# Optimization experiments

Measured on AMD Instinct MI355X. Metric: run time of the kernel, lower is better.

The kernel has to match this reference:

```python
import jax, jax.numpy as jnp
import numpy as np

DROP_P = 0.5

def setup_inputs() -> dict:
    key = jax.random.key(0)
    k_x, k_q, k_k, k_v = jax.random.split(key, 4)
    T, d_in, d_out = 4096, 1024, 1024
    x = jax.random.normal(k_x, (T, d_in), dtype=jnp.float32)
    # torch nn.Linear weights are [d_out, d_in]; init scale ~ 1/sqrt(d_in)
    s = 1.0 / np.sqrt(d_in)
    W_query = jax.random.uniform(k_q, (d_out, d_in), jnp.float32, -s, s)
    W_key = jax.random.uniform(k_k, (d_out, d_in), jnp.float32, -s, s)
    W_value = jax.random.uniform(k_v, (d_out, d_in), jnp.float32, -s, s)
    return {"x": x, "W_query": W_query, "W_key": W_key, "W_value": W_value}


def reference(x, W_query, W_key, W_value):
    # QKV projections (y = x @ W.T, matching torch Linear)
    queries = x @ W_query.T          # [T, d]
    keys = x @ W_key.T               # [T, d]
    # values = x @ W_value.T  -> feeds only the unused context_vec; dead code omitted
    d = keys.shape[-1]
    T = x.shape[0]
    attn_scores = queries @ keys.T   # [T, T]
    attn_weights = jax.nn.softmax(attn_scores / jnp.sqrt(jnp.float32(d)), axis=-1)
    # post-softmax causal masking + row renormalization (as in source)
    row = jnp.arange(T)
    causal = (row[:, None] >= row[None, :]).astype(attn_weights.dtype)  # tril of ones
    masked = attn_weights * causal
    masked_norm = masked / jnp.sum(masked, axis=-1, keepdims=True)
    # dropout(p=0.5), train mode, fixed seed
    keep = jax.random.bernoulli(jax.random.key(123), 1.0 - DROP_P, masked_norm.shape)
    return jnp.where(keep, masked_norm / (1.0 - DROP_P), 0.0)
```

## Files before the change

kernel.cpp:

```cpp
#include <hip/hip_runtime.h>
#include <hip/hip_bf16.h>


using bf16   = __bf16;
using bf16x8 = __attribute__((ext_vector_type(8))) __bf16;
using bf16x4 = __attribute__((ext_vector_type(4))) __bf16;
using f32x4  = __attribute__((ext_vector_type(4))) float;

constexpr int Tdim = 4096;
constexpr int Ddim = 1024;

__global__ __launch_bounds__(256) void k_cast_bf16(const float* __restrict__ in,
                                                   bf16* __restrict__ out, int n4) {
  int i = blockIdx.x * 256 + threadIdx.x;
  if (i >= n4) return;
  f32x4 v = reinterpret_cast<const f32x4*>(in)[i];
  bf16x4 o;
  o[0] = (bf16)v[0]; o[1] = (bf16)v[1]; o[2] = (bf16)v[2]; o[3] = (bf16)v[3];
  reinterpret_cast<bf16x4*>(out)[i] = o;
}

template<int OUTF32>
__global__ __launch_bounds__(256)
void k_gemm_bt(const bf16* __restrict__ A, const bf16* __restrict__ B,
               void* __restrict__ Cv, int M, int N, int K, int causal) {
  const int nbn = N >> 7;
  const int bm = blockIdx.x / nbn;
  const int bn = blockIdx.x - bm * nbn;
  if (causal && bn > bm) return;

  __shared__ __align__(16) bf16 As[128 * 32];
  __shared__ __align__(16) bf16 Bs[128 * 32];

  const int tid  = threadIdx.x;
  const int lane = tid & 63;
  const int wid  = tid >> 6;
  const int wr   = (wid >> 1) * 64;
  const int wc   = (wid & 1) * 64;
  const int fr   = lane & 15;
  const int ko   = (lane >> 4) * 8;

  f32x4 acc[4][4];
#pragma unroll
  for (int i = 0; i < 4; ++i)
#pragma unroll
    for (int j = 0; j < 4; ++j) acc[i][j] = (f32x4){0.f, 0.f, 0.f, 0.f};

  const bf16* Ag = A + (long)bm * 128 * K;
  const bf16* Bg = B + (long)bn * 128 * K;

  const int srow0 = tid >> 2;
  const int scol  = (tid & 3) * 8;

  for (int kt = 0; kt < K; kt += 32) {
#pragma unroll
    for (int i = 0; i < 2; ++i) {
      const int row = i * 64 + srow0;
      const int ldsbase = (i * 256 + wid * 64) * 8;
      __builtin_amdgcn_global_load_lds(
          (const __attribute__((address_space(1))) void*)(Ag + (long)row * K + kt + scol),
          (__attribute__((address_space(3))) void*)(As + ldsbase), 16, 0, 0);
      __builtin_amdgcn_global_load_lds(
          (const __attribute__((address_space(1))) void*)(Bg + (long)row * K + kt + scol),
          (__attribute__((address_space(3))) void*)(Bs + ldsbase), 16, 0, 0);
    }
    __syncthreads();

    bf16x8 av[4], bv[4];
#pragma unroll
    for (int f = 0; f < 4; ++f) {
      av[f] = *reinterpret_cast<const bf16x8*>(&As[(wr + f * 16 + fr) * 32 + ko]);
      bv[f] = *reinterpret_cast<const bf16x8*>(&Bs[(wc + f * 16 + fr) * 32 + ko]);
    }
#pragma unroll
    for (int fm = 0; fm < 4; ++fm)
#pragma unroll
      for (int fn = 0; fn < 4; ++fn)
        acc[fm][fn] = __builtin_amdgcn_mfma_f32_16x16x32_bf16(av[fm], bv[fn], acc[fm][fn], 0, 0, 0);
    __syncthreads();
  }

  const int crow0 = (lane >> 4) * 4;
  const int ccol  = lane & 15;
#pragma unroll
  for (int fm = 0; fm < 4; ++fm)
#pragma unroll
    for (int fn = 0; fn < 4; ++fn)
#pragma unroll
      for (int j = 0; j < 4; ++j) {
        const long row = (long)bm * 128 + wr + fm * 16 + crow0 + j;
        const long col = (long)bn * 128 + wc + fn * 16 + ccol;
        const float v = acc[fm][fn][j];
        if (OUTF32) ((float*)Cv)[row * N + col] = v;
        else        ((bf16*)Cv)[row * N + col] = (bf16)v;
      }
}

__device__ __forceinline__ unsigned rotl32(unsigned v, int d) {
  return (v << d) | (v >> (32 - d));
}
__device__ __forceinline__ void threefry_123(unsigned x0, unsigned x1,
                                             unsigned& o0, unsigned& o1) {
  const unsigned ks0 = 0u, ks1 = 123u;
  const unsigned ks2 = 0x1BD11BDAu ^ ks0 ^ ks1;
  x0 += ks0; x1 += ks1;
#define TF_R4(a, b, c, d)                                   \
  x0 += x1; x1 = rotl32(x1, a); x1 ^= x0;                   \
  x0 += x1; x1 = rotl32(x1, b); x1 ^= x0;                   \
  x0 += x1; x1 = rotl32(x1, c); x1 ^= x0;                   \
  x0 += x1; x1 = rotl32(x1, d); x1 ^= x0;
  TF_R4(13, 15, 26, 6);  x0 += ks1; x1 += ks2 + 1u;
  TF_R4(17, 29, 16, 24); x0 += ks2; x1 += ks0 + 2u;
  TF_R4(13, 15, 26, 6);  x0 += ks0; x1 += ks1 + 3u;
  TF_R4(17, 29, 16, 24); x0 += ks1; x1 += ks2 + 4u;
  TF_R4(13, 15, 26, 6);  x0 += ks2; x1 += ks0 + 5u;
#undef TF_R4
  o0 = x0; o1 = x1;
}

__device__ __forceinline__ bool keep_bit(unsigned i) {
  unsigned o0, o1;
  threefry_123(0u, i, o0, o1);
  return ((o0 ^ o1) & 0x80000000u) == 0u;
}

__global__ __launch_bounds__(256) void k_softmax_drop(float* __restrict__ S) {
  const int b  = blockIdx.x;
  const int r0 = b, r1 = b + (Tdim / 2);
  const int tid = threadIdx.x;
  __shared__ float redA[4], redB[4];

  float v0[8], v1[16];
  float lm0 = -3.0e38f, lm1 = -3.0e38f;
#pragma unroll
  for (int i = 0; i < 8; ++i) {
    const int c = tid + i * 256;
    v0[i] = (c <= r0) ? S[(long)r0 * Tdim + c] : -3.0e38f;
    lm0 = fmaxf(lm0, v0[i]);
  }
#pragma unroll
  for (int i = 0; i < 16; ++i) {
    const int c = tid + i * 256;
    v1[i] = (c <= r1) ? S[(long)r1 * Tdim + c] : -3.0e38f;
    lm1 = fmaxf(lm1, v1[i]);
  }
#pragma unroll
  for (int o = 32; o; o >>= 1) {
    lm0 = fmaxf(lm0, __shfl_xor(lm0, o));
    lm1 = fmaxf(lm1, __shfl_xor(lm1, o));
  }
  if ((tid & 63) == 0) { redA[tid >> 6] = lm0; redB[tid >> 6] = lm1; }
  __syncthreads();
  const float m0 = fmaxf(fmaxf(redA[0], redA[1]), fmaxf(redA[2], redA[3]));
  const float m1 = fmaxf(fmaxf(redB[0], redB[1]), fmaxf(redB[2], redB[3]));
  __syncthreads();

  constexpr float SC = 1.0f / 32.0f;
  float ls0 = 0.f, ls1 = 0.f;
#pragma unroll
  for (int i = 0; i < 8; ++i) {
    const int c = tid + i * 256;
    const float e = (c <= r0) ? __expf((v0[i] - m0) * SC) : 0.f;
    v0[i] = e; ls0 += e;
  }
#pragma unroll
  for (int i = 0; i < 16; ++i) {
    const int c = tid + i * 256;
    const float e = (c <= r1) ? __expf((v1[i] - m1) * SC) : 0.f;
    v1[i] = e; ls1 += e;
  }
#pragma unroll
  for (int o = 32; o; o >>= 1) { ls0 += __shfl_xor(ls0, o); ls1 += __shfl_xor(ls1, o); }
  if ((tid & 63) == 0) { redA[tid >> 6] = ls0; redB[tid >> 6] = ls1; }
  __syncthreads();
  const float inv0 = 2.0f / (redA[0] + redA[1] + redA[2] + redA[3]);
  const float inv1 = 2.0f / (redB[0] + redB[1] + redB[2] + redB[3]);

#pragma unroll
  for (int i = 0; i < 16; ++i) {
    const int c = tid + i * 256;
    const unsigned j = (unsigned)(r0 * Tdim + c);
    float o1v = 0.f;
    if (c <= r1 && keep_bit(j + 8388608u)) o1v = v1[i] * inv1;
    S[(long)r1 * Tdim + c] = o1v;
    float o0v = 0.f;
    if (i < 8 && c <= r0 && keep_bit(j)) o0v = v0[i & 7] * inv0;
    S[(long)r0 * Tdim + c] = o0v;
  }
}

extern "C" void kernel_launch(void* const* d_in, const int* in_sizes, int n_in,
                              void* d_out, int out_size, void* d_ws, size_t ws_size,
                              hipStream_t stream) {
  const float* x  = (const float*)d_in[0];
  const float* Wq = (const float*)d_in[1];
  const float* Wk = (const float*)d_in[2];
  float* S  = (float*)d_out;
  char* ws  = (char*)d_ws;
  bf16* xb  = (bf16*)(ws);
  bf16* wqb = (bf16*)(ws + (8l  << 20));
  bf16* wkb = (bf16*)(ws + (10l << 20));
  bf16* Qb  = (bf16*)(ws + (12l << 20));
  bf16* Kb  = (bf16*)(ws + (20l << 20));

  k_cast_bf16<<<(Tdim * Ddim / 4) / 256, 256, 0, stream>>>(x,  xb,  Tdim * Ddim / 4);
  k_cast_bf16<<<(Ddim * Ddim / 4) / 256, 256, 0, stream>>>(Wq, wqb, Ddim * Ddim / 4);
  k_cast_bf16<<<(Ddim * Ddim / 4) / 256, 256, 0, stream>>>(Wk, wkb, Ddim * Ddim / 4);

  k_gemm_bt<0><<<(Tdim / 128) * (Ddim / 128), 256, 0, stream>>>(xb, wqb, Qb, Tdim, Ddim, Ddim, 0);
  k_gemm_bt<0><<<(Tdim / 128) * (Ddim / 128), 256, 0, stream>>>(xb, wkb, Kb, Tdim, Ddim, Ddim, 0);
  k_gemm_bt<1><<<(Tdim / 128) * (Tdim / 128), 256, 0, stream>>>(Qb, Kb, (void*)S, Tdim, Tdim, Ddim, 1);

  k_softmax_drop<<<Tdim / 2, 256, 0, stream>>>(S);
}
```

Measured before the change: 215.4 us.

## Reassociate QK^T via fused weight product Wq^T Wk and double-buffer GEMM LDS

Instead of projecting both Q and K from x, the launcher forms G = Wk^T Wq (a 1024x1024 product computed with split-K and a reduce-cast), then P = x G^T, and finally S = P x^T. This drops one T x D x D projection GEMM, replacing it with a cheaper D^3 product plus a transpose-cast and a reduction kernel. The GEMM kernel also gains double-buffered LDS staging so the next tile's global-to-LDS loads overlap the current tile's MFMAs. It costs extra launches and rounds the product to bf16 at one more point, which changes the rounding of the scores.

```diff
diff --git a/kernel.cpp b/kernel.cpp
--- a/kernel.cpp
+++ b/kernel.cpp
@@ -20,17 +20,57 @@
   reinterpret_cast<bf16x4*>(out)[i] = o;
 }
 
+__global__ __launch_bounds__(256) void k_tcast(const float* __restrict__ q,
+                                               const float* __restrict__ k,
+                                               bf16* __restrict__ qt,
+                                               bf16* __restrict__ kt) {
+  const float* in = blockIdx.z ? k : q;
+  bf16* out = blockIdx.z ? kt : qt;
+  __shared__ float t[32][33];
+  const int tx = threadIdx.x & 31;
+  const int ty = threadIdx.x >> 5;
+  const int r0 = blockIdx.y * 32;
+  const int c0 = blockIdx.x * 32;
+#pragma unroll
+  for (int r = 0; r < 4; ++r)
+    t[ty * 4 + r][tx] = in[(r0 + ty * 4 + r) * Ddim + c0 + tx];
+  __syncthreads();
+#pragma unroll
+  for (int r = 0; r < 4; ++r)
+    out[(c0 + ty * 4 + r) * Ddim + r0 + tx] = (bf16)t[tx][ty * 4 + r];
+}
+
+__global__ __launch_bounds__(256) void k_redcast(const float* __restrict__ p,
+                                                 bf16* __restrict__ g) {
+  const int i = blockIdx.x * 256 + threadIdx.x;
+  f32x4 a = reinterpret_cast<const f32x4*>(p)[i];
+  f32x4 b = reinterpret_cast<const f32x4*>(p + (1 << 20))[i];
+  f32x4 c = reinterpret_cast<const f32x4*>(p + (2 << 20))[i];
+  f32x4 d = reinterpret_cast<const f32x4*>(p + (3 << 20))[i];
+  f32x4 s = a + b + c + d;
+  bf16x4 o;
+  o[0] = (bf16)s[0]; o[1] = (bf16)s[1]; o[2] = (bf16)s[2]; o[3] = (bf16)s[3];
+  reinterpret_cast<bf16x4*>(g)[i] = o;
+}
+
+__device__ __forceinline__ void gll16(const bf16* g, bf16* l) {
+  __builtin_amdgcn_global_load_lds(
+      (const __attribute__((address_space(1))) void*)g,
+      (__attribute__((address_space(3))) void*)l, 16, 0, 0);
+}
+
 template<int OUTF32>
 __global__ __launch_bounds__(256)
 void k_gemm_bt(const bf16* __restrict__ A, const bf16* __restrict__ B,
-               void* __restrict__ Cv, int M, int N, int K, int causal) {
+               void* __restrict__ Cv, int N, int lda, int ldb, int kLen,
+               long cZs, int causal) {
   const int nbn = N >> 7;
   const int bm = blockIdx.x / nbn;
   const int bn = blockIdx.x - bm * nbn;
   if (causal && bn > bm) return;
 
-  __shared__ __align__(16) bf16 As[128 * 32];
-  __shared__ __align__(16) bf16 Bs[128 * 32];
+  __shared__ __align__(16) bf16 As[2][128 * 32];
+  __shared__ __align__(16) bf16 Bs[2][128 * 32];
 
   const int tid  = threadIdx.x;
   const int lane = tid & 63;
@@ -46,39 +86,45 @@
 #pragma unroll
     for (int j = 0; j < 4; ++j) acc[i][j] = (f32x4){0.f, 0.f, 0.f, 0.f};
 
-  const bf16* Ag = A + (long)bm * 128 * K;
-  const bf16* Bg = B + (long)bn * 128 * K;
-
+  const bf16* Ag = A + (long)bm * 128 * lda;
+  const bf16* Bg = B + (long)bn * 128 * ldb;
   const int srow0 = tid >> 2;
   const int scol  = (tid & 3) * 8;
-
-  for (int kt = 0; kt < K; kt += 32) {
+  const int k0 = blockIdx.y * kLen;
+
+  auto stage = [&](int buf, int kt) {
 #pragma unroll
     for (int i = 0; i < 2; ++i) {
       const int row = i * 64 + srow0;
-      const int ldsbase = (i * 256 + wid * 64) * 8;
-      __builtin_amdgcn_global_load_lds(
-          (const __attribute__((address_space(1))) void*)(Ag + (long)row * K + kt + scol),
-          (__attribute__((address_space(3))) void*)(As + ldsbase), 16, 0, 0);
-      __builtin_amdgcn_global_load_lds(
-          (const __attribute__((address_space(1))) void*)(Bg + (long)row * K + kt + scol),
-          (__attribute__((address_space(3))) void*)(Bs + ldsbase), 16, 0, 0);
+      const int lb  = (i * 256 + wid * 64) * 8;
+      gll16(Ag + (long)row * lda + kt + scol, &As[buf][lb]);
+      gll16(Bg + (long)row * ldb + kt + scol, &Bs[buf][lb]);
     }
-    __syncthreads();
-
+  };
+  auto compute = [&](int buf) {
     bf16x8 av[4], bv[4];
 #pragma unroll
     for (int f = 0; f < 4; ++f) {
-      av[f] = *reinterpret_cast<const bf16x8*>(&As[(wr + f * 16 + fr) * 32 + ko]);
-      bv[f] = *reinterpret_cast<const bf16x8*>(&Bs[(wc + f * 16 + fr) * 32 + ko]);
+      av[f] = *reinterpret_cast<const bf16x8*>(&As[buf][(wr + f * 16 + fr) * 32 + ko]);
+      bv[f] = *reinterpret_cast<const bf16x8*>(&Bs[buf][(wc + f * 16 + fr) * 32 + ko]);
     }
 #pragma unroll
     for (int fm = 0; fm < 4; ++fm)
 #pragma unroll
       for (int fn = 0; fn < 4; ++fn)
         acc[fm][fn] = __builtin_amdgcn_mfma_f32_16x16x32_bf16(av[fm], bv[fn], acc[fm][fn], 0, 0, 0);
+  };
+
+  stage(0, k0);
+  __syncthreads();
+  int cur = 0;
+  for (int kt = 32; kt < kLen; kt += 32) {
+    stage(cur ^ 1, k0 + kt);
+    compute(cur);
     __syncthreads();
-  }
+    cur ^= 1;
+  }
+  compute(cur);
 
   const int crow0 = (lane >> 4) * 4;
   const int ccol  = lane & 15;
@@ -91,7 +137,7 @@
         const long row = (long)bm * 128 + wr + fm * 16 + crow0 + j;
         const long col = (long)bn * 128 + wc + fn * 16 + ccol;
         const float v = acc[fm][fn][j];
-        if (OUTF32) ((float*)Cv)[row * N + col] = v;
+        if (OUTF32) ((float*)Cv + (long)blockIdx.y * cZs)[row * N + col] = v;
         else        ((bf16*)Cv)[row * N + col] = (bf16)v;
       }
 }
@@ -117,7 +163,6 @@
 #undef TF_R4
   o0 = x0; o1 = x1;
 }
-
 __device__ __forceinline__ bool keep_bit(unsigned i) {
   unsigned o0, o1;
   threefry_123(0u, i, o0, o1);
@@ -195,21 +240,26 @@
   const float* x  = (const float*)d_in[0];
   const float* Wq = (const float*)d_in[1];
   const float* Wk = (const float*)d_in[2];
-  float* S  = (float*)d_out;
-  char* ws  = (char*)d_ws;
-  bf16* xb  = (bf16*)(ws);
-  bf16* wqb = (bf16*)(ws + (8l  << 20));
-  bf16* wkb = (bf16*)(ws + (10l << 20));
-  bf16* Qb  = (bf16*)(ws + (12l << 20));
-  bf16* Kb  = (bf16*)(ws + (20l << 20));
-
-  k_cast_bf16<<<(Tdim * Ddim / 4) / 256, 256, 0, stream>>>(x,  xb,  Tdim * Ddim / 4);
-  k_cast_bf16<<<(Ddim * Ddim / 4) / 256, 256, 0, stream>>>(Wq, wqb, Ddim * Ddim / 4);
-  k_cast_bf16<<<(Ddim * Ddim / 4) / 256, 256, 0, stream>>>(Wk, wkb, Ddim * Ddim / 4);
-
-  k_gemm_bt<0><<<(Tdim / 128) * (Ddim / 128), 256, 0, stream>>>(xb, wqb, Qb, Tdim, Ddim, Ddim, 0);
-  k_gemm_bt<0><<<(Tdim / 128) * (Ddim / 128), 256, 0, stream>>>(xb, wkb, Kb, Tdim, Ddim, Ddim, 0);
-  k_gemm_bt<1><<<(Tdim / 128) * (Tdim / 128), 256, 0, stream>>>(Qb, Kb, (void*)S, Tdim, Tdim, Ddim, 1);
+  float* S = (float*)d_out;
+  char* ws = (char*)d_ws;
+  bf16*  xb = (bf16*)(ws);
+  bf16*  qt = (bf16*)(ws + (8l  << 20));
+  bf16*  kt = (bf16*)(ws + (10l << 20));
+  float* Wp = (float*)(ws + (12l << 20));
+  bf16*  G  = (bf16*)(ws + (28l << 20));
+  bf16*  P  = (bf16*)(ws + (30l << 20));
+
+  k_cast_bf16<<<(Tdim * Ddim / 4) / 256, 256, 0, stream>>>(x, xb, Tdim * Ddim / 4);
+  k_tcast<<<dim3(32, 32, 2), 256, 0, stream>>>(Wq, Wk, qt, kt);
+
+  k_gemm_bt<1><<<dim3(64, 4), 256, 0, stream>>>(kt, qt, (void*)Wp, Ddim, Ddim, Ddim,
+                                                Ddim / 4, 1l << 20, 0);
+  k_redcast<<<(Ddim * Ddim / 4) / 256, 256, 0, stream>>>(Wp, G);
+
+  k_gemm_bt<0><<<dim3((Tdim / 128) * (Ddim / 128), 1), 256, 0, stream>>>(
+      xb, G, (void*)P, Ddim, Ddim, Ddim, Ddim, 0, 0);
+  k_gemm_bt<1><<<dim3((Tdim / 128) * (Tdim / 128), 1), 256, 0, stream>>>(
+      P, xb, (void*)S, Tdim, Ddim, Ddim, Ddim, 0, 1);
 
   k_softmax_drop<<<Tdim / 2, 256, 0, stream>>>(S);
 }
```

Measured after the change: 193.7 us. -10.1%, faster.
